# Optimization experiments

Hardware: AMD Instinct MI355X
Metric: run time of the kernel (lower is better)

The kernel has to match this reference:

```python
import jax, jax.numpy as jnp
import numpy as np

B, N, H = 32, 1024, 256
ALPHA = 0.2  # leaky relu slope
NEG_INF = -1e12


def setup_inputs() -> dict:
    key = jax.random.key(0)
    k1, k2, k3, k4, k5, k6 = jax.random.split(key, 6)
    inp = jax.random.normal(k1, (B, N, H), dtype=jnp.float32)
    A = (jax.random.uniform(k2, (B, N, N)) < 0.05).astype(jnp.float32)
    l = jnp.sort(jax.random.randint(k3, (B, 2), 0, N), axis=1)
    # xavier-uniform(gain=1.414) approximated; exact init values are irrelevant for correctness
    lim_w = 1.414 * np.sqrt(6.0 / (H + H))
    W_i = jax.random.uniform(k4, (H, H), minval=-lim_w, maxval=lim_w, dtype=jnp.float32)
    W_c = jax.random.uniform(k5, (H, H), minval=-lim_w, maxval=lim_w, dtype=jnp.float32)
    lim_a = 1.414 * np.sqrt(6.0 / (2 * H + 1))
    a = jax.random.uniform(k6, (2 * H, 1), minval=-lim_a, maxval=lim_a, dtype=jnp.float32)
    return {"inp": inp, "A": A, "l": l, "W_i": W_i, "W_c": W_c, "a": a}


def reference(inp, A, l, W_i, W_c, a):
    # eval mode: dropout is identity (training=False)
    n = inp.shape[1]
    h = inp.shape[2]
    Wh_i = jnp.einsum('bnh,he->bne', inp, W_i)
    Wh_c = jnp.einsum('bnh,he->bne', inp, W_c)
    # vectorized replacement of the per-batch Wh[index][i:j] = Wh_i[index][i:j] loop
    idx = jnp.arange(n)
    sel = (idx[None, :] >= l[:, 0:1]) & (idx[None, :] < l[:, 1:2])  # [B,N]
    Wh = jnp.where(sel[:, :, None], Wh_i, Wh_c)
    # additive attention scores
    Wh1 = Wh @ a[:h, :]  # [B,N,1]
    Wh2 = Wh @ a[h:, :]  # [B,N,1]
    A_ = A + jnp.eye(n, dtype=A.dtype)
    e = jax.nn.leaky_relu((Wh1 + jnp.swapaxes(Wh2, 1, 2)) * A_, ALPHA)
    att = jnp.where(A_ > 0, e, NEG_INF)
    att = jax.nn.softmax(att, axis=2)
    h_prime = jnp.einsum('bnm,bme->bne', att, Wh)
    return jax.nn.elu(h_prime)  # concat=True
```

## Files before the change

### kernel.cpp

```cpp
#include <hip/hip_runtime.h>
#include <hip/hip_bf16.h>
#include <stdint.h>

#define B_ 32
#define N_ 1024
#define H_ 256
#define PF_PITCH 520

typedef short bf16x8 __attribute__((ext_vector_type(8)));
typedef float floatx4 __attribute__((ext_vector_type(4)));

__device__ inline unsigned short f2bs(float x) {
    __hip_bfloat16 h = __float2bfloat16(x);
    return __builtin_bit_cast(unsigned short, h);
}

__global__ __launch_bounds__(256)
void k_pre(const float* __restrict__ Wi, const float* __restrict__ Wc,
           const float* __restrict__ a,
           unsigned short* __restrict__ WtFi, unsigned short* __restrict__ WtFc,
           float* __restrict__ U) {
    int t = threadIdx.x;
    if (blockIdx.x >= 32) {
        int k = blockIdx.x - 32;
        float wi = Wi[k * H_ + t];
        float wc = Wc[k * H_ + t];
        float a1 = a[t], a2 = a[H_ + t];
        float p0 = wi * a1, p1 = wc * a1, p2 = wi * a2, p3 = wc * a2;
        for (int off = 32; off; off >>= 1) {
            p0 += __shfl_xor(p0, off);
            p1 += __shfl_xor(p1, off);
            p2 += __shfl_xor(p2, off);
            p3 += __shfl_xor(p3, off);
        }
        __shared__ float red[4][4];
        int w = t >> 6;
        if ((t & 63) == 0) { red[w][0] = p0; red[w][1] = p1; red[w][2] = p2; red[w][3] = p3; }
        __syncthreads();
        if (t == 0) {
            U[0 * H_ + k] = red[0][0] + red[1][0] + red[2][0] + red[3][0];
            U[1 * H_ + k] = red[0][1] + red[1][1] + red[2][1] + red[3][1];
            U[2 * H_ + k] = red[0][2] + red[1][2] + red[2][2] + red[3][2];
            U[3 * H_ + k] = red[0][3] + red[1][3] + red[2][3] + red[3][3];
        }
        return;
    }
    __shared__ float tile[64][65];
    int mat = blockIdx.x >> 4;
    int tr = ((blockIdx.x >> 2) & 3) * 64;
    int tc = (blockIdx.x & 3) * 64;
    const float* W = mat ? Wc : Wi;
    unsigned short* WtF = mat ? WtFc : WtFi;
    int rr = t >> 2, c4 = (t & 3) * 16;
    const float* src = W + (size_t)(tr + rr) * H_ + tc + c4;
#pragma unroll
    for (int j = 0; j < 4; ++j) {
        float4 v = *reinterpret_cast<const float4*>(src + j * 4);
        tile[rr][c4 + 4 * j + 0] = v.x;
        tile[rr][c4 + 4 * j + 1] = v.y;
        tile[rr][c4 + 4 * j + 2] = v.z;
        tile[rr][c4 + 4 * j + 3] = v.w;
    }
    __syncthreads();
#pragma unroll
    for (int h = 0; h < 2; ++h) {
        int s = h * 256 + t;
        int ksl = s >> 8;
        int cl  = (s >> 6) & 3;
        int ll  = s & 63;
        int m16v = ll & 15, quadv = ll >> 4;
        int nloc = cl * 16 + m16v;
        int kb = ksl * 32 + quadv * 8;
        unsigned int pk[4];
#pragma unroll
        for (int jj = 0; jj < 4; ++jj) {
            unsigned short lo = f2bs(tile[kb + 2 * jj][nloc]);
            unsigned short hi = f2bs(tile[kb + 2 * jj + 1][nloc]);
            pk[jj] = (unsigned int)lo | ((unsigned int)hi << 16);
        }
        int ksg = (tr >> 5) + ksl;
        int cg  = (tc >> 4) + cl;
        *reinterpret_cast<uint4*>(WtF + ((size_t)(ksg * 16 + cg) * 64 + ll) * 8) =
            *reinterpret_cast<uint4*>(pk);
    }
}

__global__ __launch_bounds__(256)
void k_gemm(const float* __restrict__ inp, const int* __restrict__ l,
            const unsigned short* __restrict__ WtFi, const unsigned short* __restrict__ WtFc,
            unsigned short* __restrict__ WhF, const float* __restrict__ U,
            float* __restrict__ Wh1, float* __restrict__ Wh2) {
    __shared__ unsigned short bbuf[2][4096];
    int blk = blockIdx.x;
    int b  = blk >> 5;
    int r0 = ((blk >> 1) & 15) * 64;
    int n0 = (blk & 1) * 128;
    int t = threadIdx.x;
    int w = t >> 6;
    int lane = t & 63;
    int quad = lane >> 4, m16 = lane & 15;
    int rowb = r0 + w * 16;

    int l0 = l[2 * b], l1 = l[2 * b + 1];
    bool allI = (l0 <= r0) && (r0 + 64 <= l1);
    bool allC = (l1 <= r0) || (l0 >= r0 + 64);
    int npass = (allI || allC) ? 1 : 2;

    int row = rowb + m16;
    bool sel = (row >= l0) && (row < l1);
    const float* xrow = inp + ((size_t)(b * N_ + row)) * H_;
    const float* u1 = U + (sel ? 0 : H_);
    const float* u2 = U + 2 * H_ + (sel ? 0 : H_);
    bool doWh = (n0 == 0);
    float d1 = 0.f, d2 = 0.f;

    unsigned short* fb = WhF + (size_t)b * (N_ * H_);
    int cb = n0 >> 4;

    int j0 = rowb + quad * 4;
    int ksO = j0 >> 5;
    int laneF = m16 + 16 * ((j0 & 31) >> 3);
    int jj0 = j0 & 7;

    for (int pass = 0; pass < npass; ++pass) {
        const unsigned short* WtF =
            (npass == 1) ? (allI ? WtFi : WtFc) : (pass == 0 ? WtFi : WtFc);
        const unsigned short* gbase = WtF + cb * 512;

        floatx4 acc[8];
#pragma unroll
        for (int c = 0; c < 8; ++c) acc[c] = (floatx4){0.f, 0.f, 0.f, 0.f};

        {
            uint4 v0 = *reinterpret_cast<const uint4*>(gbase + (size_t)t * 8);
            uint4 v1 = *reinterpret_cast<const uint4*>(gbase + (size_t)(256 + t) * 8);
            *reinterpret_cast<uint4*>(&bbuf[0][t * 8]) = v0;
            *reinterpret_cast<uint4*>(&bbuf[0][(256 + t) * 8]) = v1;
        }
        for (int ks = 0; ks < 8; ++ks) {
            __syncthreads();
            uint4 v0, v1;
            if (ks < 7) {
                v0 = *reinterpret_cast<const uint4*>(gbase + (size_t)(ks + 1) * 8192 + t * 8);
                v1 = *reinterpret_cast<const uint4*>(gbase + (size_t)(ks + 1) * 8192 + (256 + t) * 8);
            }
            const float4 xa = *reinterpret_cast<const float4*>(xrow + ks * 32 + quad * 8);
            const float4 xb = *reinterpret_cast<const float4*>(xrow + ks * 32 + quad * 8 + 4);
            if (pass == 0 && doWh) {
                const float4 ua = *reinterpret_cast<const float4*>(u1 + ks * 32 + quad * 8);
                const float4 ub = *reinterpret_cast<const float4*>(u1 + ks * 32 + quad * 8 + 4);
                const float4 va = *reinterpret_cast<const float4*>(u2 + ks * 32 + quad * 8);
                const float4 vb = *reinterpret_cast<const float4*>(u2 + ks * 32 + quad * 8 + 4);
                d1 += xa.x * ua.x + xa.y * ua.y + xa.z * ua.z + xa.w * ua.w
                    + xb.x * ub.x + xb.y * ub.y + xb.z * ub.z + xb.w * ub.w;
                d2 += xa.x * va.x + xa.y * va.y + xa.z * va.z + xa.w * va.w
                    + xb.x * vb.x + xb.y * vb.y + xb.z * vb.z + xb.w * vb.w;
            }
            unsigned int pk0 = (unsigned int)f2bs(xa.x) | ((unsigned int)f2bs(xa.y) << 16);
            unsigned int pk1 = (unsigned int)f2bs(xa.z) | ((unsigned int)f2bs(xa.w) << 16);
            unsigned int pk2 = (unsigned int)f2bs(xb.x) | ((unsigned int)f2bs(xb.y) << 16);
            unsigned int pk3 = (unsigned int)f2bs(xb.z) | ((unsigned int)f2bs(xb.w) << 16);
            uint4 apk = {pk0, pk1, pk2, pk3};
            bf16x8 af = __builtin_bit_cast(bf16x8, apk);

            const unsigned short* bptr = &bbuf[ks & 1][lane * 8];
#pragma unroll
            for (int c = 0; c < 8; ++c) {
                bf16x8 bfr = *reinterpret_cast<const bf16x8*>(bptr + c * 512);
                acc[c] = __builtin_amdgcn_mfma_f32_16x16x32_bf16(af, bfr, acc[c], 0, 0, 0);
            }
            if (ks < 7) {
                *reinterpret_cast<uint4*>(&bbuf[(ks + 1) & 1][t * 8]) = v0;
                *reinterpret_cast<uint4*>(&bbuf[(ks + 1) & 1][(256 + t) * 8]) = v1;
            }
        }
        __syncthreads();

#pragma unroll
        for (int c = 0; c < 8; ++c) {
            size_t base = ((size_t)((ksO * 16 + cb + c) * 64) + laneF) * 8 + jj0;
            if (npass == 1) {
                unsigned int lo = (unsigned int)f2bs(acc[c][0]) | ((unsigned int)f2bs(acc[c][1]) << 16);
                unsigned int hi = (unsigned int)f2bs(acc[c][2]) | ((unsigned int)f2bs(acc[c][3]) << 16);
                uint2 v = {lo, hi};
                *reinterpret_cast<uint2*>(fb + base) = v;
            } else {
                bool want[4]; bool all = true, none = true;
#pragma unroll
                for (int r = 0; r < 4; ++r) {
                    int j = j0 + r;
                    bool s2 = (j >= l0) && (j < l1);
                    want[r] = (pass == 0) ? s2 : !s2;
                    all = all && want[r]; none = none && !want[r];
                }
                if (all) {
                    unsigned int lo = (unsigned int)f2bs(acc[c][0]) | ((unsigned int)f2bs(acc[c][1]) << 16);
                    unsigned int hi = (unsigned int)f2bs(acc[c][2]) | ((unsigned int)f2bs(acc[c][3]) << 16);
                    uint2 v = {lo, hi};
                    *reinterpret_cast<uint2*>(fb + base) = v;
                } else if (!none) {
#pragma unroll
                    for (int r = 0; r < 4; ++r)
                        if (want[r]) fb[base + r] = f2bs(acc[c][r]);
                }
            }
        }
    }

    if (doWh) {
        d1 += __shfl_xor(d1, 16); d1 += __shfl_xor(d1, 32);
        d2 += __shfl_xor(d2, 16); d2 += __shfl_xor(d2, 32);
        if (quad == 0) {
            Wh1[b * N_ + rowb + m16] = d1;
            Wh2[b * N_ + rowb + m16] = d2;
        }
    }
}

__global__ __launch_bounds__(256, 4)
void k_attn(const float* __restrict__ A, const float* __restrict__ Wh1,
            const float* __restrict__ Wh2, const unsigned short* __restrict__ WhF,
            float* __restrict__ out) {
    __shared__ unsigned short pfrag[32 * PF_PITCH];
    int t = threadIdx.x, w = t >> 6, lane = t & 63;
    int quad = lane >> 4, m16 = lane & 15;
    int bi = blockIdx.x;
    int b = (bi & 7) * 4 + ((bi >> 3) >> 6);
    int tile = (bi >> 3) & 63;
    int rowbase = tile * 16;

    const float* Wh2b = Wh2 + b * N_;
    float4 w2v[4];
#pragma unroll
    for (int ch = 0; ch < 4; ++ch)
        w2v[ch] = *reinterpret_cast<const float4*>(Wh2b + ch * 256 + lane * 4);

    int ksl = lane >> 3;
    int q2 = (lane & 7) >> 1;
    int jj0 = (lane & 1) * 4;

#pragma unroll
    for (int q = 0; q < 4; ++q) {
        int m = w * 4 + q;
        int i = rowbase + m;
        float wh1 = Wh1[b * N_ + i];
        const float* Arow = A + ((size_t)(b * N_ + i)) * N_;
        int s = m + 16 * q2;
        int sw = s ^ ((s >> 3) & 7);
        int sls = sw * 8 + jj0;
#pragma unroll
        for (int ch = 0; ch < 4; ++ch) {
            float4 av = *reinterpret_cast<const float4*>(Arow + ch * 256 + lane * 4);
            if ((i >> 2) == (ch * 64 + lane)) ((float*)&av)[i & 3] += 1.0f;
            float aa[4] = {av.x, av.y, av.z, av.w};
            float ww[4] = {w2v[ch].x, w2v[ch].y, w2v[ch].z, w2v[ch].w};
            float p[4];
#pragma unroll
            for (int c = 0; c < 4; ++c) {
                float e  = (wh1 + ww[c]) * aa[c];
                float lv = fmaxf(e, 0.2f * e);
                p[c] = aa[c] > 0.f ? __expf(lv) : 0.f;
            }
            unsigned int lo = (unsigned int)f2bs(p[0]) | ((unsigned int)f2bs(p[1]) << 16);
            unsigned int hi = (unsigned int)f2bs(p[2]) | ((unsigned int)f2bs(p[3]) << 16);
            uint2 v = {lo, hi};
            int ks = ch * 8 + ksl;
            *reinterpret_cast<uint2*>(pfrag + ks * PF_PITCH + sls) = v;
        }
    }
    __syncthreads();

    const unsigned short* WB = WhF + (size_t)b * (N_ * H_);
    int rs = (lane ^ ((lane >> 3) & 7)) * 8;
    unsigned short oneb = f2bs(1.0f);
    bf16x8 bones = {(short)oneb, (short)oneb, (short)oneb, (short)oneb,
                    (short)oneb, (short)oneb, (short)oneb, (short)oneb};
    floatx4 acc[4], rsum = (floatx4){0.f, 0.f, 0.f, 0.f};
#pragma unroll
    for (int cc = 0; cc < 4; ++cc) acc[cc] = (floatx4){0.f, 0.f, 0.f, 0.f};
#pragma unroll 4
    for (int ks = 0; ks < 32; ++ks) {
        bf16x8 af = *reinterpret_cast<const bf16x8*>(pfrag + ks * PF_PITCH + rs);
        rsum = __builtin_amdgcn_mfma_f32_16x16x32_bf16(af, bones, rsum, 0, 0, 0);
#pragma unroll
        for (int cc = 0; cc < 4; ++cc) {
            int c = w * 4 + cc;
            bf16x8 bfv = *reinterpret_cast<const bf16x8*>(
                WB + ((size_t)((ks * 16 + c) * 64 + lane)) * 8);
            acc[cc] = __builtin_amdgcn_mfma_f32_16x16x32_bf16(af, bfv, acc[cc], 0, 0, 0);
        }
    }

    float inv[4];
#pragma unroll
    for (int r = 0; r < 4; ++r) inv[r] = 1.0f / rsum[r];
#pragma unroll
    for (int cc = 0; cc < 4; ++cc) {
        int col = (w * 4 + cc) * 16 + m16;
#pragma unroll
        for (int r = 0; r < 4; ++r) {
            int m = quad * 4 + r;
            float v = acc[cc][r] * inv[r];
            v = v > 0.f ? v : __expf(v) - 1.0f;
            out[((size_t)(b * N_ + rowbase + m)) * H_ + col] = v;
        }
    }
}

extern "C" void kernel_launch(void* const* d_in, const int* in_sizes, int n_in,
                              void* d_out, int out_size, void* d_ws, size_t ws_size,
                              hipStream_t stream) {
    const float* inp = (const float*)d_in[0];
    const float* A   = (const float*)d_in[1];
    const int*   l   = (const int*)d_in[2];
    const float* Wi  = (const float*)d_in[3];
    const float* Wc  = (const float*)d_in[4];
    const float* a   = (const float*)d_in[5];
    float* out = (float*)d_out;

    char* ws = (char*)d_ws;
    size_t off = 0;
    unsigned short* WhF  = (unsigned short*)(ws + off); off += (size_t)B_ * N_ * H_ * 2;
    float* Wh1 = (float*)(ws + off); off += (size_t)B_ * N_ * 4;
    float* Wh2 = (float*)(ws + off); off += (size_t)B_ * N_ * 4;
    float* U   = (float*)(ws + off); off += 4 * H_ * 4;
    unsigned short* WtFi = (unsigned short*)(ws + off); off += (size_t)H_ * H_ * 2;
    unsigned short* WtFc = (unsigned short*)(ws + off); off += (size_t)H_ * H_ * 2;

    k_pre<<<288, 256, 0, stream>>>(Wi, Wc, a, WtFi, WtFc, U);
    k_gemm<<<B_ * 16 * 2, 256, 0, stream>>>(inp, l, WtFi, WtFc, WhF, U, Wh1, Wh2);
    k_attn<<<B_ * (N_ / 16), 256, 0, stream>>>(A, Wh1, Wh2, WhF, out);
}
```

Measured before the change: 287.3 us.

## Pack adjacency into bitmasks inside the GEMM kernel and read bits in attention

k_gemm now also reads the fp32 adjacency matrix and turns each row into 64-bit ballot bitmasks, which it writes to a workspace buffer. k_attn reads these bitmasks instead of the full fp32 A rows. It rebuilds A+I as 0/1 values, adding the self-loop on the diagonal. The goal is to move the large A stream into the GEMM kernel, where it can overlap with MFMA work, and to shrink what the attention kernel loads. It adds a small bitmask write and read, and it relies on A being binary.

```diff
diff --git a/kernel.cpp b/kernel.cpp
--- a/kernel.cpp
+++ b/kernel.cpp
@@ -89,7 +89,8 @@
 void k_gemm(const float* __restrict__ inp, const int* __restrict__ l,
             const unsigned short* __restrict__ WtFi, const unsigned short* __restrict__ WtFc,
             unsigned short* __restrict__ WhF, const float* __restrict__ U,
-            float* __restrict__ Wh1, float* __restrict__ Wh2) {
+            float* __restrict__ Wh1, float* __restrict__ Wh2,
+            const float* __restrict__ Aglob, unsigned long long* __restrict__ bits) {
     __shared__ unsigned short bbuf[2][4096];
     int blk = blockIdx.x;
     int b  = blk >> 5;
@@ -100,6 +101,7 @@
     int lane = t & 63;
     int quad = lane >> 4, m16 = lane & 15;
     int rowb = r0 + w * 16;
+    int rbase = (blk & 31) * 32;
 
     int l0 = l[2 * b], l1 = l[2 * b + 1];
     bool allI = (l0 <= r0) && (r0 + 64 <= l1);
@@ -139,6 +141,25 @@
         }
         for (int ks = 0; ks < 8; ++ks) {
             __syncthreads();
+            if (pass == 0) {
+                int ra = rbase + ks * 4 + w;
+                const float* ar = Aglob + ((size_t)(b * N_) + ra) * N_;
+                unsigned long long* bp = bits + ((size_t)(b * N_) + ra) * 16;
+#pragma unroll
+                for (int ch = 0; ch < 4; ++ch) {
+                    float4 av = *reinterpret_cast<const float4*>(ar + ch * 256 + lane * 4);
+                    unsigned long long m0 = __ballot(av.x > 0.f);
+                    unsigned long long m1 = __ballot(av.y > 0.f);
+                    unsigned long long m2 = __ballot(av.z > 0.f);
+                    unsigned long long m3 = __ballot(av.w > 0.f);
+                    if (lane == 0) {
+                        bp[ch * 4 + 0] = m0;
+                        bp[ch * 4 + 1] = m1;
+                        bp[ch * 4 + 2] = m2;
+                        bp[ch * 4 + 3] = m3;
+                    }
+                }
+            }
             uint4 v0, v1;
             if (ks < 7) {
                 v0 = *reinterpret_cast<const uint4*>(gbase + (size_t)(ks + 1) * 8192 + t * 8);
@@ -218,7 +239,7 @@
 }
 
 __global__ __launch_bounds__(256, 4)
-void k_attn(const float* __restrict__ A, const float* __restrict__ Wh1,
+void k_attn(const unsigned long long* __restrict__ bits, const float* __restrict__ Wh1,
             const float* __restrict__ Wh2, const unsigned short* __restrict__ WhF,
             float* __restrict__ out) {
     __shared__ unsigned short pfrag[32 * PF_PITCH];
@@ -244,22 +265,26 @@
         int m = w * 4 + q;
         int i = rowbase + m;
         float wh1 = Wh1[b * N_ + i];
-        const float* Arow = A + ((size_t)(b * N_ + i)) * N_;
+        const unsigned long long* bp = bits + ((size_t)(b * N_ + i)) * 16;
         int s = m + 16 * q2;
         int sw = s ^ ((s >> 3) & 7);
         int sls = sw * 8 + jj0;
 #pragma unroll
         for (int ch = 0; ch < 4; ++ch) {
-            float4 av = *reinterpret_cast<const float4*>(Arow + ch * 256 + lane * 4);
-            if ((i >> 2) == (ch * 64 + lane)) ((float*)&av)[i & 3] += 1.0f;
-            float aa[4] = {av.x, av.y, av.z, av.w};
+            unsigned long long bm0 = bp[ch * 4 + 0];
+            unsigned long long bm1 = bp[ch * 4 + 1];
+            unsigned long long bm2 = bp[ch * 4 + 2];
+            unsigned long long bm3 = bp[ch * 4 + 3];
+            unsigned long long bmv[4] = {bm0, bm1, bm2, bm3};
             float ww[4] = {w2v[ch].x, w2v[ch].y, w2v[ch].z, w2v[ch].w};
             float p[4];
 #pragma unroll
             for (int c = 0; c < 4; ++c) {
-                float e  = (wh1 + ww[c]) * aa[c];
+                float a_ = (float)((bmv[c] >> lane) & 1ull);
+                if (ch * 256 + lane * 4 + c == i) a_ += 1.0f;
+                float e  = (wh1 + ww[c]) * a_;
                 float lv = fmaxf(e, 0.2f * e);
-                p[c] = aa[c] > 0.f ? __expf(lv) : 0.f;
+                p[c] = a_ > 0.f ? __expf(lv) : 0.f;
             }
             unsigned int lo = (unsigned int)f2bs(p[0]) | ((unsigned int)f2bs(p[1]) << 16);
             unsigned int hi = (unsigned int)f2bs(p[2]) | ((unsigned int)f2bs(p[3]) << 16);
@@ -326,8 +351,9 @@
     float* U   = (float*)(ws + off); off += 4 * H_ * 4;
     unsigned short* WtFi = (unsigned short*)(ws + off); off += (size_t)H_ * H_ * 2;
     unsigned short* WtFc = (unsigned short*)(ws + off); off += (size_t)H_ * H_ * 2;
+    unsigned long long* bits = (unsigned long long*)(ws + off); off += (size_t)B_ * N_ * 16 * 8;
 
     k_pre<<<288, 256, 0, stream>>>(Wi, Wc, a, WtFi, WtFc, U);
-    k_gemm<<<B_ * 16 * 2, 256, 0, stream>>>(inp, l, WtFi, WtFc, WhF, U, Wh1, Wh2);
-    k_attn<<<B_ * (N_ / 16), 256, 0, stream>>>(A, Wh1, Wh2, WhF, out);
-}
+    k_gemm<<<B_ * 16 * 2, 256, 0, stream>>>(inp, l, WtFi, WtFc, WhF, U, Wh1, Wh2, A, bits);
+    k_attn<<<B_ * (N_ / 16), 256, 0, stream>>>(bits, Wh1, Wh2, WhF, out);
+}
```

New measurement: 364.1 us. 1.27x slower.
